# Optimization experiments

Hardware: AMD Instinct MI355X
Metric: run time of the kernel (lower is better)

Reference implementation:

```python
import jax, jax.numpy as jnp
import numpy as np

TOP_K = 4
N_GROUP = 4
TOPK_GROUP = 2
ROUTED_SCALING = 1.0


def setup_inputs() -> dict:
    key = jax.random.key(0)
    k1, k2, k3, k4, k5 = jax.random.split(key, 5)
    B, S, H, I, E = 1, 2048, 1024, 512, 16
    hidden_states = jax.random.normal(k1, (B, S, H), dtype=jnp.float32)
    # router weight (kaiming-uniform-like scale)
    gate_weight = jax.random.normal(k2, (E, H), dtype=jnp.float32) * (1.0 / np.sqrt(H))
    e_bias = jnp.zeros((E,), dtype=jnp.float32)  # e_score_correction_bias buffer
    gate_proj = jax.random.normal(k3, (E, I, H), dtype=jnp.float32) * 0.02
    up_proj = jax.random.normal(k4, (E, I, H), dtype=jnp.float32) * 0.02
    down_proj = jax.random.normal(k5, (E, H, I), dtype=jnp.float32) * 0.02
    return {
        "hidden_states": hidden_states,
        "gate_weight": gate_weight,
        "e_bias": e_bias,
        "gate_proj": gate_proj,
        "up_proj": up_proj,
        "down_proj": down_proj,
    }


def _route(x_flat, gate_weight, e_bias):
    # x_flat: [T, H]
    T = x_flat.shape[0]
    E = gate_weight.shape[0]
    logits = jnp.einsum("th,eh->te", x_flat, gate_weight)
    scores = jax.nn.sigmoid(logits)                      # [T, E]
    scores_for_choice = scores + e_bias[None, :]
    # group scores = sum of top-2 expert scores within each group
    grp = scores_for_choice.reshape(T, N_GROUP, E // N_GROUP)
    top2, _ = jax.lax.top_k(grp, 2)
    group_scores = top2.sum(axis=-1)                     # [T, G]
    _, group_idx = jax.lax.top_k(group_scores, TOPK_GROUP)
    group_mask = jax.nn.one_hot(group_idx, N_GROUP, dtype=scores.dtype).sum(axis=1)  # [T, G]
    score_mask = jnp.repeat(group_mask, E // N_GROUP, axis=1)                        # [T, E]
    tmp_scores = jnp.where(score_mask > 0, scores_for_choice, 0.0)
    _, topk_idx = jax.lax.top_k(tmp_scores, TOP_K)       # [T, K]
    topk_weight = jnp.take_along_axis(scores, topk_idx, axis=1)
    denom = topk_weight.sum(axis=-1, keepdims=True) + 1e-20
    topk_weight = topk_weight / denom * ROUTED_SCALING
    return topk_idx, topk_weight


def reference(hidden_states, gate_weight, e_bias, gate_proj, up_proj, down_proj):
    B, S, H = hidden_states.shape
    E = gate_proj.shape[0]
    x = hidden_states.reshape(-1, H).astype(jnp.float32)  # [T, H]
    topk_idx, topk_weight = _route(x, gate_weight, e_bias)
    # combine weights per (token, expert): sum over the k slots selecting e
    combine = (jax.nn.one_hot(topk_idx, E, dtype=x.dtype) * topk_weight[..., None]).sum(axis=1)  # [T, E]
    # dense expert MLP (mathematically equal to gather-compute-scatter since
    # non-selected experts receive zero combine weight)
    g = jnp.einsum("th,eih->tei", x, gate_proj)
    u = jnp.einsum("th,eih->tei", x, up_proj)
    act = jax.nn.silu(g) * u                              # [T, E, I]
    expert_out = jnp.einsum("tei,ehi->teh", act, down_proj)
    y = jnp.einsum("teh,te->th", expert_out, combine)
    return y.reshape(B, S, H)
```

## Files before the change

kernel.cpp:

```cpp
#include <hip/hip_runtime.h>
#include <hip/hip_bf16.h>

typedef __attribute__((ext_vector_type(8))) short bf16x8;
typedef __attribute__((ext_vector_type(4))) float f32x4;

#define T_TOK 2048
#define HD 1024
#define ID 512
#define NE 16
#define TOPK 4
#define BK 64
#define WELEM (HD*ID*NE)
#define CPAD 16

__device__ __forceinline__ unsigned pk2(float a, float b) {
    return __builtin_amdgcn_perm(__float_as_uint(b), __float_as_uint(a),
                                 0x07060302u);
}
__device__ __forceinline__ bf16x8 cvt8(const float* __restrict__ p) {
    float4 a = *(const float4*)p;
    float4 b = *(const float4*)(p + 4);
    union { bf16x8 v; unsigned u[4]; } r;
    r.u[0] = pk2(a.x, a.y); r.u[1] = pk2(a.z, a.w);
    r.u[2] = pk2(b.x, b.y); r.u[3] = pk2(b.z, b.w);
    return r.v;
}
__device__ __forceinline__ short f2bf(float f) {
    unsigned u = __float_as_uint(f);
    return (short)((u + 0x7fffu + ((u >> 16) & 1u)) >> 16);
}
__device__ __forceinline__ float bf2f(short s) {
    return __uint_as_float(((unsigned)(unsigned short)s) << 16);
}
__device__ __forceinline__ void load_lds16(const short* g, short* l) {
    __builtin_amdgcn_global_load_lds(
        (const __attribute__((address_space(1))) unsigned*)g,
        (__attribute__((address_space(3))) unsigned*)l, 16, 0, 0);
}

#define MFMA_BF16 __builtin_amdgcn_mfma_f32_16x16x32_bf16

__global__ __launch_bounds__(256) void conv_k(
        const float* __restrict__ s0, short* __restrict__ d0,
        const float* __restrict__ s1, short* __restrict__ d1,
        const float* __restrict__ s2, short* __restrict__ d2,
        int* __restrict__ counts) {
    if (blockIdx.x == 0 && blockIdx.y == 0)
        counts[threadIdx.x] = 0;
    const float* src = (blockIdx.y == 0) ? s0 : (blockIdx.y == 1) ? s1 : s2;
    short* dst       = (blockIdx.y == 0) ? d0 : (blockIdx.y == 1) ? d1 : d2;
    size_t i = ((size_t)blockIdx.x * 256 + threadIdx.x) * 8;
    union { bf16x8 v; uint4 q; } r;
    r.v = cvt8(src + i);
    *(uint4*)(dst + i) = r.q;
}

__global__ __launch_bounds__(256) void router_k(
        const float* __restrict__ x, const float* __restrict__ gw,
        const float* __restrict__ eb,
        int* __restrict__ tk_idx, float* __restrict__ tk_w,
        short* __restrict__ xb) {
    int wid  = (blockIdx.x * 256 + threadIdx.x) >> 6;
    int lane = threadIdx.x & 63;

    const float* xr = x + (size_t)wid * HD + lane * 16;
    float xv[16];
#pragma unroll
    for (int c = 0; c < 4; c++) {
        float4 v = *(const float4*)(xr + c * 4);
        xv[4 * c] = v.x; xv[4 * c + 1] = v.y; xv[4 * c + 2] = v.z; xv[4 * c + 3] = v.w;
    }
    {
        union { uint4 q; unsigned u[4]; } w0, w1;
        w0.u[0] = pk2(xv[0], xv[1]);  w0.u[1] = pk2(xv[2], xv[3]);
        w0.u[2] = pk2(xv[4], xv[5]);  w0.u[3] = pk2(xv[6], xv[7]);
        w1.u[0] = pk2(xv[8], xv[9]);  w1.u[1] = pk2(xv[10], xv[11]);
        w1.u[2] = pk2(xv[12], xv[13]); w1.u[3] = pk2(xv[14], xv[15]);
        short* d = xb + ((size_t)wid << 10) + lane * 16;
        *(uint4*)d = w0.q;
        *(uint4*)(d + 8) = w1.q;
    }

    float logits[NE];
#pragma unroll
    for (int e = 0; e < NE; e++) {
        const float* gr = gw + e * HD + lane * 16;
        float p = 0.f;
#pragma unroll
        for (int c = 0; c < 4; c++) {
            float4 v = *(const float4*)(gr + c * 4);
            p += xv[4 * c] * v.x + xv[4 * c + 1] * v.y +
                 xv[4 * c + 2] * v.z + xv[4 * c + 3] * v.w;
        }
#pragma unroll
        for (int s = 32; s > 0; s >>= 1) p += __shfl_xor(p, s, 64);
        logits[e] = p;
    }

    float scores[NE], sc[NE];
#pragma unroll
    for (int e = 0; e < NE; e++) {
        scores[e] = 1.f / (1.f + __expf(-logits[e]));
        sc[e] = scores[e] + eb[e];
    }

    float gs[4];
#pragma unroll
    for (int g = 0; g < 4; g++) {
        float a = sc[4 * g], b = sc[4 * g + 1], c = sc[4 * g + 2], d = sc[4 * g + 3];
        float h1 = fmaxf(a, b), l1 = fminf(a, b);
        float h2 = fmaxf(c, d), l2 = fminf(c, d);
        gs[g] = fmaxf(h1, h2) + fmaxf(fminf(h1, h2), fmaxf(l1, l2));
    }
    int g0 = 0; float b0 = gs[0];
#pragma unroll
    for (int g = 1; g < 4; g++) if (gs[g] > b0) { b0 = gs[g]; g0 = g; }
    int g1 = -1; float b1 = -1e30f;
#pragma unroll
    for (int g = 0; g < 4; g++) if (g != g0 && gs[g] > b1) { b1 = gs[g]; g1 = g; }

    int taken = 0;
    int bid[TOPK]; float bsc[TOPK]; float wsum = 0.f;
#pragma unroll
    for (int k = 0; k < TOPK; k++) {
        float bv = -1e30f; int bi = 0; float bs = 0.f;
#pragma unroll
        for (int e = 0; e < NE; e++) {
            int grp = e >> 2;
            bool ok = ((grp == g0) || (grp == g1)) && !((taken >> e) & 1);
            if (ok && sc[e] > bv) { bv = sc[e]; bi = e; bs = scores[e]; }
        }
        taken |= (1 << bi);
        bid[k] = bi; bsc[k] = bs; wsum += bs;
    }
    if (lane == 0) {
        float inv = 1.0f / (wsum + 1e-20f);
#pragma unroll
        for (int k = 0; k < TOPK; k++) {
            tk_idx[wid * TOPK + k] = bid[k];
            tk_w[wid * TOPK + k]   = bsc[k] * inv;
        }
    }
}

__global__ __launch_bounds__(256) void assign_k(
        const int* __restrict__ tk_idx,
        int* __restrict__ counts, int* __restrict__ tok_list,
        int* __restrict__ pair_slot) {
    int p = blockIdx.x * 256 + threadIdx.x;
    int e = tk_idx[p];
    int slot = atomicAdd(&counts[e * CPAD], 1);
    tok_list[e * T_TOK + slot] = p >> 2;
    pair_slot[p] = slot;
}

__global__ __launch_bounds__(256) void gemm1_k(
        const short* __restrict__ xb,
        const short* __restrict__ gpb,
        const short* __restrict__ upb,
        const int* __restrict__ counts,
        const int* __restrict__ tok_list,
        short* __restrict__ act) {
    __shared__ short xs[2][128 * BK];
    __shared__ short gs[2][64 * BK];
    __shared__ short us[2][64 * BK];
    __shared__ int   tok_s[128];

    int e = blockIdx.z;
    int cnt = counts[e * CPAD];
    int base = blockIdx.y * 128;
    if (base >= cnt) return;
    int off = 0;
#pragma unroll
    for (int q = 0; q < NE; q++) if (q < e) off += counts[q * CPAD];
    int arow0 = off + base;

    int tid = threadIdx.x;
    if (tid < 128) {
        int s = base + tid;
        tok_s[tid] = (s < cnt) ? tok_list[e * T_TOK + s] : tok_list[e * T_TOK];
    }
    __syncthreads();

    int wv = tid >> 6, lane = tid & 63;
    int qd = lane >> 4, l16 = lane & 15;
    int wm = (wv >> 1) * 64, wn = (wv & 1) * 32;
    int nb0 = blockIdx.x * 64;
    const short* gp = gpb + (size_t)e * ID * HD + (size_t)nb0 * HD;
    const short* up = upb + (size_t)e * ID * HD + (size_t)nb0 * HD;

    const short* xsg[4]; short* xld[4];
#pragma unroll
    for (int i = 0; i < 4; i++) {
        int idx = i * 256 + tid, r = idx >> 3, c = idx & 7;
        xsg[i] = xb + ((size_t)tok_s[r] << 10) + (((c ^ r) & 7) << 3);
        xld[i] = &xs[0][(i * 256 + wv * 64) * 8];
    }
    const short* gsg[2]; const short* usg[2]; short* gld[2]; short* uld[2];
#pragma unroll
    for (int i = 0; i < 2; i++) {
        int idx = i * 256 + tid, r = idx >> 3, c = idx & 7;
        size_t so = (size_t)r * HD + (((c ^ r) & 7) << 3);
        gsg[i] = gp + so;
        usg[i] = up + so;
        gld[i] = &gs[0][(i * 256 + wv * 64) * 8];
        uld[i] = &us[0][(i * 256 + wv * 64) * 8];
    }

    f32x4 accg[4][2] = {};
    f32x4 accu[4][2] = {};

    auto STAGE = [&](int kp, int b) {
#pragma unroll
        for (int i = 0; i < 4; i++)
            load_lds16(xsg[i] + kp, xld[i] + b * (128 * BK));
#pragma unroll
        for (int i = 0; i < 2; i++) {
            load_lds16(gsg[i] + kp, gld[i] + b * (64 * BK));
            load_lds16(usg[i] + kp, uld[i] + b * (64 * BK));
        }
    };
    auto COMPUTE = [&](int b) {
        const short* xsb = xs[b];
        const short* gsb = gs[b];
        const short* usb = us[b];
#pragma unroll
        for (int ks = 0; ks < 2; ks++) {
            int cb = ks * 4 + qd;
            bf16x8 af[4], bg[2], bu[2];
#pragma unroll
            for (int i = 0; i < 4; i++) {
                int r = wm + i * 16 + l16;
                af[i] = *(const bf16x8*)&xsb[(r << 6) + (((cb ^ r) & 7) << 3)];
            }
#pragma unroll
            for (int j = 0; j < 2; j++) {
                int r = wn + j * 16 + l16;
                int lo = (r << 6) + (((cb ^ r) & 7) << 3);
                bg[j] = *(const bf16x8*)&gsb[lo];
                bu[j] = *(const bf16x8*)&usb[lo];
            }
#pragma unroll
            for (int i = 0; i < 4; i++)
#pragma unroll
                for (int j = 0; j < 2; j++) {
                    accg[i][j] = MFMA_BF16(af[i], bg[j], accg[i][j], 0, 0, 0);
                    accu[i][j] = MFMA_BF16(af[i], bu[j], accu[i][j], 0, 0, 0);
                }
        }
    };

    constexpr int NP = HD / BK;
    STAGE(0, 0);
    auto STEP = [&](int p, int b) {
        if (p + 1 < NP) {
            STAGE((p + 1) * BK, b ^ 1);
            asm volatile("s_waitcnt vmcnt(8)" ::: "memory");
        } else {
            asm volatile("s_waitcnt vmcnt(0)" ::: "memory");
        }
        __builtin_amdgcn_s_barrier();
        asm volatile("" ::: "memory");
        COMPUTE(b);
        asm volatile("" ::: "memory");
        __builtin_amdgcn_s_barrier();
    };
#pragma unroll 1
    for (int p = 0; p < NP; p += 2) { STEP(p, 0); STEP(p + 1, 1); }

#pragma unroll
    for (int i = 0; i < 4; i++)
#pragma unroll
        for (int j = 0; j < 2; j++)
#pragma unroll
            for (int r = 0; r < 4; r++) {
                int m = wm + i * 16 + qd * 4 + r;
                if (base + m < cnt) {
                    float g = accg[i][j][r], u = accu[i][j][r];
                    float a = g / (1.f + __expf(-g)) * u;
                    act[(size_t)(arow0 + m) * ID + nb0 + wn + j * 16 + l16] = f2bf(a);
                }
            }
}

__global__ __launch_bounds__(256) void gemm2_k(
        const short* __restrict__ act,
        const short* __restrict__ dpb,
        const int* __restrict__ counts,
        short* __restrict__ yexp) {
    __shared__ short as_[2][128 * BK];
    __shared__ short ds_[2][128 * BK];

    int e = blockIdx.z;
    int cnt = counts[e * CPAD];
    int base = blockIdx.y * 128;
    if (base >= cnt) return;
    int off = 0;
#pragma unroll
    for (int q = 0; q < NE; q++) if (q < e) off += counts[q * CPAD];
    int arow0 = off + base;

    int tid = threadIdx.x;
    int wv = tid >> 6, lane = tid & 63;
    int qd = lane >> 4, l16 = lane & 15;
    int wm = (wv >> 1) * 64, wn = (wv & 1) * 64;
    int hb0 = blockIdx.x * 128;
    const short* dp = dpb + (size_t)e * HD * ID + (size_t)hb0 * ID;

    const short* asg[4]; const short* dsg[4]; short* ald[4]; short* dld[4];
#pragma unroll
    for (int i = 0; i < 4; i++) {
        int idx = i * 256 + tid, r = idx >> 3, c = idx & 7;
        int sw = ((c ^ r) & 7) << 3;
        asg[i] = act + (size_t)(arow0 + r) * ID + sw;
        dsg[i] = dp + (size_t)r * ID + sw;
        ald[i] = &as_[0][(i * 256 + wv * 64) * 8];
        dld[i] = &ds_[0][(i * 256 + wv * 64) * 8];
    }

    f32x4 acc[4][4] = {};

    auto STAGE = [&](int kp, int b) {
#pragma unroll
        for (int i = 0; i < 4; i++) {
            load_lds16(asg[i] + kp, ald[i] + b * (128 * BK));
            load_lds16(dsg[i] + kp, dld[i] + b * (128 * BK));
        }
    };
    auto COMPUTE = [&](int b) {
        const short* asb = as_[b];
        const short* dsb = ds_[b];
#pragma unroll
        for (int ks = 0; ks < 2; ks++) {
            int cb = ks * 4 + qd;
            bf16x8 af[4], bd[4];
#pragma unroll
            for (int i = 0; i < 4; i++) {
                int r = wm + i * 16 + l16;
                af[i] = *(const bf16x8*)&asb[(r << 6) + (((cb ^ r) & 7) << 3)];
                int r2 = wn + i * 16 + l16;
                bd[i] = *(const bf16x8*)&dsb[(r2 << 6) + (((cb ^ r2) & 7) << 3)];
            }
#pragma unroll
            for (int i = 0; i < 4; i++)
#pragma unroll
                for (int j = 0; j < 4; j++)
                    acc[i][j] = MFMA_BF16(af[i], bd[j], acc[i][j], 0, 0, 0);
        }
    };

    constexpr int NP = ID / BK;
    STAGE(0, 0);
    auto STEP = [&](int p, int b) {
        if (p + 1 < NP) {
            STAGE((p + 1) * BK, b ^ 1);
            asm volatile("s_waitcnt vmcnt(8)" ::: "memory");
        } else {
            asm volatile("s_waitcnt vmcnt(0)" ::: "memory");
        }
        __builtin_amdgcn_s_barrier();
        asm volatile("" ::: "memory");
        COMPUTE(b);
        asm volatile("" ::: "memory");
        __builtin_amdgcn_s_barrier();
    };
#pragma unroll 1
    for (int p = 0; p < NP; p += 2) { STEP(p, 0); STEP(p + 1, 1); }

#pragma unroll
    for (int i = 0; i < 4; i++)
#pragma unroll
        for (int j = 0; j < 4; j++)
#pragma unroll
            for (int r = 0; r < 4; r++) {
                int m = wm + i * 16 + qd * 4 + r;
                if (base + m < cnt)
                    yexp[(size_t)(arow0 + m) * HD + hb0 + wn + j * 16 + l16] =
                        f2bf(acc[i][j][r]);
            }
}

__global__ __launch_bounds__(256) void combine_k(
        const short* __restrict__ yexp,
        const int* __restrict__ counts,
        const int* __restrict__ tk_idx, const float* __restrict__ tk_w,
        const int* __restrict__ pair_slot,
        float* __restrict__ out) {
    __shared__ int offs_s[NE];
    if (threadIdx.x == 0) {
        int a = 0;
#pragma unroll
        for (int e = 0; e < NE; e++) { offs_s[e] = a; a += counts[e * CPAD]; }
    }
    __syncthreads();

    int t = blockIdx.x * 2 + (threadIdx.x >> 7);
    int i = threadIdx.x & 127;
    float acc[8] = {};
#pragma unroll
    for (int k = 0; k < TOPK; k++) {
        int p = t * TOPK + k;
        int e = tk_idx[p];
        int row = offs_s[e] + pair_slot[p];
        float w = tk_w[p];
        bf16x8 v = *(const bf16x8*)(yexp + (size_t)row * HD + i * 8);
#pragma unroll
        for (int j = 0; j < 8; j++) acc[j] += w * bf2f(v[j]);
    }
    float4 o0 = {acc[0], acc[1], acc[2], acc[3]};
    float4 o1 = {acc[4], acc[5], acc[6], acc[7]};
    float* d = out + (size_t)t * HD + i * 8;
    *(float4*)d = o0;
    *(float4*)(d + 4) = o1;
}

extern "C" void kernel_launch(void* const* d_in, const int* in_sizes, int n_in,
                              void* d_out, int out_size, void* d_ws, size_t ws_size,
                              hipStream_t stream) {
    const float* x  = (const float*)d_in[0];
    const float* gw = (const float*)d_in[1];
    const float* eb = (const float*)d_in[2];
    const float* gp = (const float*)d_in[3];
    const float* up = (const float*)d_in[4];
    const float* dp = (const float*)d_in[5];

    short* gpb = (short*)d_ws;
    short* upb = gpb + WELEM;
    short* dpb = upb + WELEM;
    short* xb  = dpb + WELEM;
    short* act = xb + (size_t)T_TOK * HD;
    int* counts    = (int*)(act + (size_t)(T_TOK * TOPK + 128) * ID);
    int* tok_list  = counts + NE * CPAD;
    int* pair_slot = tok_list + NE * T_TOK;
    int* tk_idx    = pair_slot + T_TOK * TOPK;
    float* tk_w    = (float*)(tk_idx + T_TOK * TOPK);
    short* yexp = gpb;

    conv_k<<<dim3(WELEM / 8 / 256, 3), 256, 0, stream>>>(gp, gpb, up, upb,
                                                         dp, dpb, counts);
    router_k<<<T_TOK / 4, 256, 0, stream>>>(x, gw, eb, tk_idx, tk_w, xb);
    assign_k<<<T_TOK * TOPK / 256, 256, 0, stream>>>(tk_idx, counts,
                                                     tok_list, pair_slot);
    gemm1_k<<<dim3(ID / 64, T_TOK / 128, NE), 256, 0, stream>>>(
        xb, gpb, upb, counts, tok_list, act);
    gemm2_k<<<dim3(HD / 128, T_TOK / 128, NE), 256, 0, stream>>>(
        act, dpb, counts, yexp);
    combine_k<<<T_TOK / 2, 256, 0, stream>>>(yexp, counts, tk_idx, tk_w,
                                             pair_slot, (float*)d_out);
}
```

Baseline: 238.4 us.

## Halve GEMM K-tile to 32 with new swizzle and reorder grid dims

Both expert GEMM kernels shrink the K-step staged into LDS from 64 to 32, which halves shared memory per block and roughly doubles the number of pipeline stages. The XOR swizzle is adjusted to the 4-chunk row width, and the wait counts are updated to match the smaller number of loads per stage. The grid is also reordered so the expert index runs along x and the token block along z, which changes the order blocks are dispatched and spreads work across experts earlier. The smaller LDS footprint may allow more resident blocks, at the cost of more barriers and less compute per synchronisation.

```diff
diff --git a/kernel.cpp b/kernel.cpp
--- a/kernel.cpp
+++ b/kernel.cpp
@@ -9,7 +9,7 @@
 #define ID 512
 #define NE 16
 #define TOPK 4
-#define BK 64
+#define BK 32
 #define WELEM (HD*ID*NE)
 #define CPAD 16
 
@@ -166,9 +166,9 @@
     __shared__ short us[2][64 * BK];
     __shared__ int   tok_s[128];
 
-    int e = blockIdx.z;
+    int e = blockIdx.x;
     int cnt = counts[e * CPAD];
-    int base = blockIdx.y * 128;
+    int base = blockIdx.z * 128;
     if (base >= cnt) return;
     int off = 0;
 #pragma unroll
@@ -185,69 +185,62 @@
     int wv = tid >> 6, lane = tid & 63;
     int qd = lane >> 4, l16 = lane & 15;
     int wm = (wv >> 1) * 64, wn = (wv & 1) * 32;
-    int nb0 = blockIdx.x * 64;
+    int nb0 = blockIdx.y * 64;
     const short* gp = gpb + (size_t)e * ID * HD + (size_t)nb0 * HD;
     const short* up = upb + (size_t)e * ID * HD + (size_t)nb0 * HD;
 
-    const short* xsg[4]; short* xld[4];
-#pragma unroll
-    for (int i = 0; i < 4; i++) {
-        int idx = i * 256 + tid, r = idx >> 3, c = idx & 7;
-        xsg[i] = xb + ((size_t)tok_s[r] << 10) + (((c ^ r) & 7) << 3);
+    const short* xsg[2]; short* xld[2];
+#pragma unroll
+    for (int i = 0; i < 2; i++) {
+        int idx = i * 256 + tid, r = idx >> 2, c = idx & 3;
+        int f = (r >> 1) & 3;
+        xsg[i] = xb + ((size_t)tok_s[r] << 10) + ((c ^ f) << 3);
         xld[i] = &xs[0][(i * 256 + wv * 64) * 8];
     }
-    const short* gsg[2]; const short* usg[2]; short* gld[2]; short* uld[2];
-#pragma unroll
-    for (int i = 0; i < 2; i++) {
-        int idx = i * 256 + tid, r = idx >> 3, c = idx & 7;
-        size_t so = (size_t)r * HD + (((c ^ r) & 7) << 3);
-        gsg[i] = gp + so;
-        usg[i] = up + so;
-        gld[i] = &gs[0][(i * 256 + wv * 64) * 8];
-        uld[i] = &us[0][(i * 256 + wv * 64) * 8];
+    const short* gsg; const short* usg; short* gld; short* uld;
+    {
+        int r = tid >> 2, c = tid & 3;
+        int f = (r >> 1) & 3;
+        size_t so = (size_t)r * HD + ((c ^ f) << 3);
+        gsg = gp + so;
+        usg = up + so;
+        gld = &gs[0][(wv * 64) * 8];
+        uld = &us[0][(wv * 64) * 8];
     }
 
     f32x4 accg[4][2] = {};
     f32x4 accu[4][2] = {};
 
     auto STAGE = [&](int kp, int b) {
-#pragma unroll
-        for (int i = 0; i < 4; i++)
-            load_lds16(xsg[i] + kp, xld[i] + b * (128 * BK));
-#pragma unroll
-        for (int i = 0; i < 2; i++) {
-            load_lds16(gsg[i] + kp, gld[i] + b * (64 * BK));
-            load_lds16(usg[i] + kp, uld[i] + b * (64 * BK));
-        }
+        load_lds16(xsg[0] + kp, xld[0] + b * (128 * BK));
+        load_lds16(xsg[1] + kp, xld[1] + b * (128 * BK));
+        load_lds16(gsg + kp, gld + b * (64 * BK));
+        load_lds16(usg + kp, uld + b * (64 * BK));
     };
     auto COMPUTE = [&](int b) {
         const short* xsb = xs[b];
         const short* gsb = gs[b];
         const short* usb = us[b];
-#pragma unroll
-        for (int ks = 0; ks < 2; ks++) {
-            int cb = ks * 4 + qd;
-            bf16x8 af[4], bg[2], bu[2];
-#pragma unroll
-            for (int i = 0; i < 4; i++) {
-                int r = wm + i * 16 + l16;
-                af[i] = *(const bf16x8*)&xsb[(r << 6) + (((cb ^ r) & 7) << 3)];
+        bf16x8 af[4], bg[2], bu[2];
+#pragma unroll
+        for (int i = 0; i < 4; i++) {
+            int r = wm + i * 16 + l16;
+            af[i] = *(const bf16x8*)&xsb[r * BK + ((qd ^ ((r >> 1) & 3)) << 3)];
+        }
+#pragma unroll
+        for (int j = 0; j < 2; j++) {
+            int r = wn + j * 16 + l16;
+            int lo = r * BK + ((qd ^ ((r >> 1) & 3)) << 3);
+            bg[j] = *(const bf16x8*)&gsb[lo];
+            bu[j] = *(const bf16x8*)&usb[lo];
+        }
+#pragma unroll
+        for (int i = 0; i < 4; i++)
+#pragma unroll
+            for (int j = 0; j < 2; j++) {
+                accg[i][j] = MFMA_BF16(af[i], bg[j], accg[i][j], 0, 0, 0);
+                accu[i][j] = MFMA_BF16(af[i], bu[j], accu[i][j], 0, 0, 0);
             }
-#pragma unroll
-            for (int j = 0; j < 2; j++) {
-                int r = wn + j * 16 + l16;
-                int lo = (r << 6) + (((cb ^ r) & 7) << 3);
-                bg[j] = *(const bf16x8*)&gsb[lo];
-                bu[j] = *(const bf16x8*)&usb[lo];
-            }
-#pragma unroll
-            for (int i = 0; i < 4; i++)
-#pragma unroll
-                for (int j = 0; j < 2; j++) {
-                    accg[i][j] = MFMA_BF16(af[i], bg[j], accg[i][j], 0, 0, 0);
-                    accu[i][j] = MFMA_BF16(af[i], bu[j], accu[i][j], 0, 0, 0);
-                }
-        }
     };
 
     constexpr int NP = HD / BK;
@@ -255,7 +248,7 @@
     auto STEP = [&](int p, int b) {
         if (p + 1 < NP) {
             STAGE((p + 1) * BK, b ^ 1);
-            asm volatile("s_waitcnt vmcnt(8)" ::: "memory");
+            asm volatile("s_waitcnt vmcnt(4)" ::: "memory");
         } else {
             asm volatile("s_waitcnt vmcnt(0)" ::: "memory");
         }
@@ -291,9 +284,9 @@
     __shared__ short as_[2][128 * BK];
     __shared__ short ds_[2][128 * BK];
 
-    int e = blockIdx.z;
+    int e = blockIdx.x;
     int cnt = counts[e * CPAD];
-    int base = blockIdx.y * 128;
+    int base = blockIdx.z * 128;
     if (base >= cnt) return;
     int off = 0;
 #pragma unroll
@@ -304,14 +297,15 @@
     int wv = tid >> 6, lane = tid & 63;
     int qd = lane >> 4, l16 = lane & 15;
     int wm = (wv >> 1) * 64, wn = (wv & 1) * 64;
-    int hb0 = blockIdx.x * 128;
+    int hb0 = blockIdx.y * 128;
     const short* dp = dpb + (size_t)e * HD * ID + (size_t)hb0 * ID;
 
-    const short* asg[4]; const short* dsg[4]; short* ald[4]; short* dld[4];
-#pragma unroll
-    for (int i = 0; i < 4; i++) {
-        int idx = i * 256 + tid, r = idx >> 3, c = idx & 7;
-        int sw = ((c ^ r) & 7) << 3;
+    const short* asg[2]; const short* dsg[2]; short* ald[2]; short* dld[2];
+#pragma unroll
+    for (int i = 0; i < 2; i++) {
+        int idx = i * 256 + tid, r = idx >> 2, c = idx & 3;
+        int f = (r >> 1) & 3;
+        int sw = (c ^ f) << 3;
         asg[i] = act + (size_t)(arow0 + r) * ID + sw;
         dsg[i] = dp + (size_t)r * ID + sw;
         ald[i] = &as_[0][(i * 256 + wv * 64) * 8];
@@ -321,32 +315,27 @@
     f32x4 acc[4][4] = {};
 
     auto STAGE = [&](int kp, int b) {
-#pragma unroll
-        for (int i = 0; i < 4; i++) {
-            load_lds16(asg[i] + kp, ald[i] + b * (128 * BK));
-            load_lds16(dsg[i] + kp, dld[i] + b * (128 * BK));
-        }
+        load_lds16(asg[0] + kp, ald[0] + b * (128 * BK));
+        load_lds16(asg[1] + kp, ald[1] + b * (128 * BK));
+        load_lds16(dsg[0] + kp, dld[0] + b * (128 * BK));
+        load_lds16(dsg[1] + kp, dld[1] + b * (128 * BK));
     };
     auto COMPUTE = [&](int b) {
         const short* asb = as_[b];
         const short* dsb = ds_[b];
-#pragma unroll
-        for (int ks = 0; ks < 2; ks++) {
-            int cb = ks * 4 + qd;
-            bf16x8 af[4], bd[4];
-#pragma unroll
-            for (int i = 0; i < 4; i++) {
-                int r = wm + i * 16 + l16;
-                af[i] = *(const bf16x8*)&asb[(r << 6) + (((cb ^ r) & 7) << 3)];
-                int r2 = wn + i * 16 + l16;
-                bd[i] = *(const bf16x8*)&dsb[(r2 << 6) + (((cb ^ r2) & 7) << 3)];
-            }
-#pragma unroll
-            for (int i = 0; i < 4; i++)
-#pragma unroll
-                for (int j = 0; j < 4; j++)
-                    acc[i][j] = MFMA_BF16(af[i], bd[j], acc[i][j], 0, 0, 0);
-        }
+        bf16x8 af[4], bd[4];
+#pragma unroll
+        for (int i = 0; i < 4; i++) {
+            int r = wm + i * 16 + l16;
+            af[i] = *(const bf16x8*)&asb[r * BK + ((qd ^ ((r >> 1) & 3)) << 3)];
+            int r2 = wn + i * 16 + l16;
+            bd[i] = *(const bf16x8*)&dsb[r2 * BK + ((qd ^ ((r2 >> 1) & 3)) << 3)];
+        }
+#pragma unroll
+        for (int i = 0; i < 4; i++)
+#pragma unroll
+            for (int j = 0; j < 4; j++)
+                acc[i][j] = MFMA_BF16(af[i], bd[j], acc[i][j], 0, 0, 0);
     };
 
     constexpr int NP = ID / BK;
@@ -354,7 +343,7 @@
     auto STEP = [&](int p, int b) {
         if (p + 1 < NP) {
             STAGE((p + 1) * BK, b ^ 1);
-            asm volatile("s_waitcnt vmcnt(8)" ::: "memory");
+            asm volatile("s_waitcnt vmcnt(4)" ::: "memory");
         } else {
             asm volatile("s_waitcnt vmcnt(0)" ::: "memory");
         }
@@ -441,9 +430,9 @@
     router_k<<<T_TOK / 4, 256, 0, stream>>>(x, gw, eb, tk_idx, tk_w, xb);
     assign_k<<<T_TOK * TOPK / 256, 256, 0, stream>>>(tk_idx, counts,
                                                      tok_list, pair_slot);
-    gemm1_k<<<dim3(ID / 64, T_TOK / 128, NE), 256, 0, stream>>>(
+    gemm1_k<<<dim3(NE, ID / 64, T_TOK / 128), 256, 0, stream>>>(
         xb, gpb, upb, counts, tok_list, act);
-    gemm2_k<<<dim3(HD / 128, T_TOK / 128, NE), 256, 0, stream>>>(
+    gemm2_k<<<dim3(NE, HD / 128, T_TOK / 128), 256, 0, stream>>>(
         act, dpb, counts, yexp);
     combine_k<<<T_TOK / 2, 256, 0, stream>>>(yexp, counts, tk_idx, tk_w,
                                              pair_slot, (float*)d_out);
```

Measured after the change: 222.4 us. 6.7% less time.
